# Kernel optimization log

Measured on AMD Instinct MI355X. Metric: run time of the kernel, lower is better.

Reference implementation:

```python
import jax, jax.numpy as jnp
import numpy as np

NEG_SLOPE = 0.01  # torch.nn.LeakyReLU default


def setup_inputs() -> dict:
    key = jax.random.key(0)
    ks = jax.random.split(key, 9)
    B, S, F1, F2, N, M, E, L = 2, 256, 512, 512, 20000, 2, 320000, 3
    x = jax.random.normal(ks[0], (B, S, F1), dtype=jnp.float32)
    nodes = jax.random.normal(ks[1], (N, M, F2), dtype=jnp.float32)
    edge_index = jax.random.randint(ks[2], (2, E), 0, N, dtype=jnp.int32)
    Wp = jax.random.normal(ks[3], (F1, F2), dtype=jnp.float32) * 0.02  # torch Linear weight [out,in]
    bp = jax.random.normal(ks[4], (F1,), dtype=jnp.float32) * 0.02
    gcn_W = jax.random.normal(ks[5], (L, S, S), dtype=jnp.float32) * 0.05  # stored as [in,out]
    gcn_b = jax.random.normal(ks[6], (L, S), dtype=jnp.float32) * 0.02
    w_bp = jax.random.normal(ks[7], (S,), dtype=jnp.float32) * 0.05
    b_bp = jax.random.normal(ks[8], (1,), dtype=jnp.float32) * 0.02
    return {"x": x, "nodes": nodes, "edge_index": edge_index, "Wp": Wp, "bp": bp,
            "gcn_W": gcn_W, "gcn_b": gcn_b, "w_bp": w_bp, "b_bp": b_bp}


def reference(x, nodes, edge_index, Wp, bp, gcn_W, gcn_b, w_bp, b_bp):
    # Eval mode: dropout layers are identity.
    N = nodes.shape[0]
    L = gcn_W.shape[0]
    proj = nodes @ Wp.T + bp                         # [N, M, F1]
    score = jnp.einsum('bsk,nmk->bsn', x, proj)      # sum over M and F1 -> [B, S, N]
    h = score.transpose(0, 2, 1)                     # beliefs [B, N, S]

    # GCN normalization with self-loops: D^{-1/2} (A + I) D^{-1/2}
    src, dst = edge_index[0], edge_index[1]
    loop = jnp.arange(N, dtype=edge_index.dtype)
    row = jnp.concatenate([src, loop])               # message sources
    col = jnp.concatenate([dst, loop])               # message targets
    deg = jnp.zeros((N,), dtype=h.dtype).at[col].add(1.0)
    dinv = deg ** -0.5                               # deg >= 1 due to self-loops
    norm = dinv[row] * dinv[col]                     # [E+N]

    for l in range(L):
        hw = h @ gcn_W[l]                            # [B, N, S]
        msg = hw[:, row, :] * norm[None, :, None]    # gather + scale
        agg = jnp.zeros_like(hw).at[:, col, :].add(msg) + gcn_b[l]
        h = jax.nn.leaky_relu(agg, NEG_SLOPE)

    # belief_projection: Linear(S, 1) then squeeze -> [B, N]
    return h @ w_bp + b_bp[0]
```

## Files before the change

kernel.cpp:

```cpp
#include <hip/hip_runtime.h>
#include <cstddef>
#include <cstdint>

#define NN 20000

typedef short frag16 __attribute__((ext_vector_type(8)));
typedef float f32x4 __attribute__((ext_vector_type(4)));

__device__ inline unsigned short f32_to_bf16(float f) {
    uint32_t u = __float_as_uint(f);
    u += 0x7FFFu + ((u >> 16) & 1u);
    return (unsigned short)(u >> 16);
}

__device__ inline float4 dec4(uint2 v) {
    float4 r;
    r.x = __uint_as_float(v.x << 16);
    r.y = __uint_as_float(v.x & 0xffff0000u);
    r.z = __uint_as_float(v.y << 16);
    r.w = __uint_as_float(v.y & 0xffff0000u);
    return r;
}

__global__ __launch_bounds__(256) void prep(
    const float* __restrict__ nodes, const float* __restrict__ x,
    const float* __restrict__ gcn_W, const float* __restrict__ bp,
    const int* __restrict__ src, const int* __restrict__ dst,
    unsigned short* __restrict__ nsum16, unsigned short* __restrict__ WT,
    float* __restrict__ Tf, float* __restrict__ cvec,
    int* __restrict__ cnt, int* __restrict__ csr, int E)
{
    __shared__ __align__(16) char shmem[8704];
    const int blk = blockIdx.x, tid = threadIdx.x;
    const int eb = (E + 255) >> 8;

    if (blk < eb) {
        int e = blk * 256 + tid;
        if (e < E) {
            int d = dst[e];
            int pos = atomicAdd(&cnt[d], 1);
            if (pos < 64) csr[(d << 6) + pos] = src[e];
        }
    } else if (blk < eb + 64) {
        float* As = (float*)shmem;
        float* Bs = As + 1024;
        int t = blk - eb;
        int b = t >> 5, rem = t & 31;
        int s0 = (rem >> 3) * 64, f0 = (rem & 7) * 64;
        const float* W1 = gcn_W;
        const float* xb = x + (size_t)b * 256 * 512;
        int kk = tid >> 4, c4 = (tid & 15) << 2;
        int tm = tid >> 4, tn = tid & 15;
        float acc[4][4] = {};
        for (int k0 = 0; k0 < 256; k0 += 16) {
            float4 av = *(const float4*)(W1 + (size_t)(k0 + kk) * 256 + s0 + c4);
            float4 bv = *(const float4*)(xb + (size_t)(k0 + kk) * 512 + f0 + c4);
            __syncthreads();
            *(float4*)&As[kk * 64 + c4] = av;
            *(float4*)&Bs[kk * 64 + c4] = bv;
            __syncthreads();
            #pragma unroll
            for (int k = 0; k < 16; ++k) {
                float a[4], bb[4];
                *(float4*)a  = *(const float4*)&As[k * 64 + (tm << 2)];
                *(float4*)bb = *(const float4*)&Bs[k * 64 + (tn << 2)];
                #pragma unroll
                for (int i = 0; i < 4; ++i)
                    #pragma unroll
                    for (int j = 0; j < 4; ++j) acc[i][j] += a[i] * bb[j];
            }
        }
        #pragma unroll
        for (int i = 0; i < 4; ++i) {
            int row = b * 256 + s0 + (tm << 2) + i;
            *(float4*)(Tf + (size_t)row * 512 + f0 + (tn << 2)) =
                make_float4(acc[i][0], acc[i][1], acc[i][2], acc[i][3]);
        }
    } else if (blk < eb + 64 + 2512) {
        int g = (blk - eb - 64) * 256 + tid;
        int n = g >> 5, c = (g & 31) << 4;
        uint4 o0, o1;
        if (n < NN) {
            const float* r0 = nodes + (size_t)n * 1024 + c;
            const float* r1 = r0 + 512;
            float4 a0 = *(const float4*)(r0 + 0),  a1 = *(const float4*)(r0 + 4);
            float4 a2 = *(const float4*)(r0 + 8),  a3 = *(const float4*)(r0 + 12);
            float4 b0 = *(const float4*)(r1 + 0),  b1 = *(const float4*)(r1 + 4);
            float4 b2 = *(const float4*)(r1 + 8),  b3 = *(const float4*)(r1 + 12);
            o0.x = ((uint32_t)f32_to_bf16(a0.y + b0.y) << 16) | f32_to_bf16(a0.x + b0.x);
            o0.y = ((uint32_t)f32_to_bf16(a0.w + b0.w) << 16) | f32_to_bf16(a0.z + b0.z);
            o0.z = ((uint32_t)f32_to_bf16(a1.y + b1.y) << 16) | f32_to_bf16(a1.x + b1.x);
            o0.w = ((uint32_t)f32_to_bf16(a1.w + b1.w) << 16) | f32_to_bf16(a1.z + b1.z);
            o1.x = ((uint32_t)f32_to_bf16(a2.y + b2.y) << 16) | f32_to_bf16(a2.x + b2.x);
            o1.y = ((uint32_t)f32_to_bf16(a2.w + b2.w) << 16) | f32_to_bf16(a2.z + b2.z);
            o1.z = ((uint32_t)f32_to_bf16(a3.y + b3.y) << 16) | f32_to_bf16(a3.x + b3.x);
            o1.w = ((uint32_t)f32_to_bf16(a3.w + b3.w) << 16) | f32_to_bf16(a3.z + b3.z);
        } else {
            o0 = make_uint4(0, 0, 0, 0); o1 = o0;
        }
        *(uint4*)(nsum16 + (size_t)n * 512 + c) = o0;
        *(uint4*)(nsum16 + (size_t)n * 512 + c + 8) = o1;
    } else if (blk < eb + 64 + 2512 + 32) {
        unsigned short (*tsh)[68] = (unsigned short(*)[68])shmem;
        int t = blk - eb - 64 - 2512;
        int l = t >> 4, rem = t & 15;
        int c0 = (rem & 3) * 64, r0 = (rem >> 2) * 64;
        const float* inp = gcn_W + (size_t)(l + 1) * 65536;
        unsigned short* outp = WT + (size_t)l * 65536;
        int tx = tid & 15, ty = tid >> 4;
        #pragma unroll
        for (int rr = 0; rr < 4; ++rr) {
            int r = ty * 4 + rr;
            float4 v = *(const float4*)(inp + (size_t)(r0 + r) * 256 + c0 + tx * 4);
            tsh[tx * 4 + 0][r] = f32_to_bf16(v.x);
            tsh[tx * 4 + 1][r] = f32_to_bf16(v.y);
            tsh[tx * 4 + 2][r] = f32_to_bf16(v.z);
            tsh[tx * 4 + 3][r] = f32_to_bf16(v.w);
        }
        __syncthreads();
        #pragma unroll
        for (int cc = 0; cc < 4; ++cc) {
            int c = ty * 4 + cc;
            ushort4 o = *(ushort4*)&tsh[c][tx * 4];
            *(ushort4*)(outp + (size_t)(c0 + c) * 256 + r0 + tx * 4) = o;
        }
    } else {
        int row = (blk - eb - 64 - 2512 - 32) * 4 + (tid >> 6);
        int lane = tid & 63;
        const float* xr = x + (size_t)row * 512;
        float s = 0.f;
        #pragma unroll
        for (int k = 0; k < 512; k += 64) s += xr[k + lane] * bp[k + lane];
        #pragma unroll
        for (int off = 32; off; off >>= 1) s += __shfl_down(s, off);
        if (lane == 0) cvec[row] = 2.0f * s;
    }
}

__global__ __launch_bounds__(256) void mid(
    const float* __restrict__ Tf, const float* __restrict__ Wp,
    const float* __restrict__ gcn_W, const float* __restrict__ cvec,
    unsigned short* __restrict__ Ub, float* __restrict__ cb2)
{
    const int blk = blockIdx.x, tid = threadIdx.x;
    if (blk >= 64) {
        int idx = (blk - 64) * 256 + tid;
        int b = idx >> 8, s = idx & 255;
        float sum = 0.f;
        for (int sp = 0; sp < 256; ++sp)
            sum += gcn_W[(size_t)sp * 256 + s] * cvec[b * 256 + sp];
        cb2[idx] = sum;
        return;
    }
    __shared__ float As[16][68];
    __shared__ float Bs[16][64];
    int bm = (blk >> 3) * 64, bn = (blk & 7) * 64;
    int arow = tid >> 2, acol = (tid & 3) << 2;
    int brow = tid >> 4, bcol = (tid & 15) << 2;
    int tm = tid >> 4, tn = tid & 15;
    float acc[4][4] = {};
    for (int k0 = 0; k0 < 512; k0 += 16) {
        float4 av = *(const float4*)(Tf + (size_t)(bm + arow) * 512 + k0 + acol);
        float4 bv = *(const float4*)(Wp + (size_t)(k0 + brow) * 512 + bn + bcol);
        __syncthreads();
        As[acol + 0][arow] = av.x; As[acol + 1][arow] = av.y;
        As[acol + 2][arow] = av.z; As[acol + 3][arow] = av.w;
        *(float4*)&Bs[brow][bcol] = bv;
        __syncthreads();
        #pragma unroll
        for (int k = 0; k < 16; ++k) {
            float a[4], b[4];
            *(float4*)a = *(const float4*)&As[k][tm << 2];
            *(float4*)b = *(const float4*)&Bs[k][tn << 2];
            #pragma unroll
            for (int i = 0; i < 4; ++i)
                #pragma unroll
                for (int j = 0; j < 4; ++j) acc[i][j] += a[i] * b[j];
        }
    }
    #pragma unroll
    for (int i = 0; i < 4; ++i) {
        int row = bm + (tm << 2) + i;
        ushort4 o;
        o.x = f32_to_bf16(acc[i][0]); o.y = f32_to_bf16(acc[i][1]);
        o.z = f32_to_bf16(acc[i][2]); o.w = f32_to_bf16(acc[i][3]);
        *(ushort4*)(Ub + (size_t)row * 512 + bn + (tn << 2)) = o;
    }
}

__global__ __launch_bounds__(256) void mgemm(
    const unsigned short* __restrict__ A, const unsigned short* __restrict__ BT,
    int K, int N, int mode,
    const float* __restrict__ cb2, const int* __restrict__ cnt,
    unsigned short* __restrict__ C)
{
    __shared__ __align__(16) unsigned short As[128 * 32];
    __shared__ __align__(16) unsigned short Bs[128 * 32];
    const int bm = blockIdx.y * 128, bn = blockIdx.x * 128;
    const int tid = threadIdx.x;
    const int lane = tid & 63, w = tid >> 6;
    const int wm = (w >> 1) << 6, wn = (w & 1) << 6;
    const int r = lane & 15, q = lane >> 4;

    f32x4 acc[4][4] = {};

    for (int k0 = 0; k0 < K; k0 += 32) {
        __syncthreads();
        #pragma unroll
        for (int t = 0; t < 2; ++t) {
            int c = t * 256 + w * 64 + lane;
            int row = c >> 2, col = (c & 3) << 3;
            __builtin_amdgcn_global_load_lds(
                (const __attribute__((address_space(1))) void*)(A + (size_t)(bm + row) * K + k0 + col),
                (__attribute__((address_space(3))) void*)(As + (size_t)(t * 256 + w * 64) * 8),
                16, 0, 0);
            __builtin_amdgcn_global_load_lds(
                (const __attribute__((address_space(1))) void*)(BT + (size_t)(bn + row) * K + k0 + col),
                (__attribute__((address_space(3))) void*)(Bs + (size_t)(t * 256 + w * 64) * 8),
                16, 0, 0);
        }
        __syncthreads();
        frag16 af[4], bf[4];
        #pragma unroll
        for (int i = 0; i < 4; ++i)
            af[i] = *(const frag16*)(As + ((wm + i * 16 + r) << 5) + (q << 3));
        #pragma unroll
        for (int j = 0; j < 4; ++j)
            bf[j] = *(const frag16*)(Bs + ((wn + j * 16 + r) << 5) + (q << 3));
        #pragma unroll
        for (int i = 0; i < 4; ++i)
            #pragma unroll
            for (int j = 0; j < 4; ++j)
                acc[i][j] = __builtin_amdgcn_mfma_f32_16x16x32_bf16(af[i], bf[j], acc[i][j], 0, 0, 0);
    }

    #pragma unroll
    for (int i = 0; i < 4; ++i) {
        #pragma unroll
        for (int rg = 0; rg < 4; ++rg) {
            int m = bm + wm + i * 16 + (q << 2) + rg;
            float sc;
            int b2 = 0, node = m;
            if (mode == 1) {
                int nc = m > NN - 1 ? NN - 1 : m;
                sc = rsqrtf((float)cnt[nc] + 1.0f);
            } else {
                b2 = m >= NN;
                node = m - b2 * NN;
                int nc = node > NN - 1 ? NN - 1 : node;
                sc = rsqrtf((float)cnt[nc] + 1.0f);
                if (node > 20095) node = 20095;
            }
            #pragma unroll
            for (int j = 0; j < 4; ++j) {
                int n = bn + wn + j * 16 + r;
                if (mode == 1) {
                    float v = (acc[i][j][rg] + cb2[n]) * sc;
                    C[(size_t)m * 512 + n] = f32_to_bf16(v);
                } else {
                    float v = acc[i][j][rg] * sc;
                    C[(size_t)node * 512 + (b2 << 8) + n] = f32_to_bf16(v);
                }
            }
        }
    }
}

__global__ __launch_bounds__(256) void aggregate_s(
    const unsigned short* __restrict__ hw, const int* __restrict__ cnt,
    const int* __restrict__ csr, const float* __restrict__ bias,
    unsigned short* __restrict__ hout,
    const float* __restrict__ w_bp, const float* __restrict__ b_bp,
    float* __restrict__ out)
{
    int n = blockIdx.x * 4 + (threadIdx.x >> 6);
    int b = blockIdx.y;
    int lane = threadIdx.x & 63;
    const unsigned short* rowp = hw + (b << 8) + (lane << 2);

    int deg = cnt[n]; if (deg > 64) deg = 64;
    int myidx = csr[(n << 6) + lane];

    float4 acc = dec4(*(const uint2*)(rowp + (size_t)n * 512));
    int e = 0;
    for (; e + 8 <= deg; e += 8) {
        int s0 = __shfl(myidx, e + 0), s1 = __shfl(myidx, e + 1);
        int s2 = __shfl(myidx, e + 2), s3 = __shfl(myidx, e + 3);
        int s4 = __shfl(myidx, e + 4), s5 = __shfl(myidx, e + 5);
        int s6 = __shfl(myidx, e + 6), s7 = __shfl(myidx, e + 7);
        uint2 u0 = *(const uint2*)(rowp + (size_t)s0 * 512);
        uint2 u1 = *(const uint2*)(rowp + (size_t)s1 * 512);
        uint2 u2 = *(const uint2*)(rowp + (size_t)s2 * 512);
        uint2 u3 = *(const uint2*)(rowp + (size_t)s3 * 512);
        uint2 u4 = *(const uint2*)(rowp + (size_t)s4 * 512);
        uint2 u5 = *(const uint2*)(rowp + (size_t)s5 * 512);
        uint2 u6 = *(const uint2*)(rowp + (size_t)s6 * 512);
        uint2 u7 = *(const uint2*)(rowp + (size_t)s7 * 512);
        float4 f0 = dec4(u0), f1 = dec4(u1), f2 = dec4(u2), f3 = dec4(u3);
        float4 f4 = dec4(u4), f5 = dec4(u5), f6 = dec4(u6), f7 = dec4(u7);
        acc.x += ((f0.x + f1.x) + (f2.x + f3.x)) + ((f4.x + f5.x) + (f6.x + f7.x));
        acc.y += ((f0.y + f1.y) + (f2.y + f3.y)) + ((f4.y + f5.y) + (f6.y + f7.y));
        acc.z += ((f0.z + f1.z) + (f2.z + f3.z)) + ((f4.z + f5.z) + (f6.z + f7.z));
        acc.w += ((f0.w + f1.w) + (f2.w + f3.w)) + ((f4.w + f5.w) + (f6.w + f7.w));
    }
    if (e + 4 <= deg) {
        int s0 = __shfl(myidx, e + 0), s1 = __shfl(myidx, e + 1);
        int s2 = __shfl(myidx, e + 2), s3 = __shfl(myidx, e + 3);
        uint2 u0 = *(const uint2*)(rowp + (size_t)s0 * 512);
        uint2 u1 = *(const uint2*)(rowp + (size_t)s1 * 512);
        uint2 u2 = *(const uint2*)(rowp + (size_t)s2 * 512);
        uint2 u3 = *(const uint2*)(rowp + (size_t)s3 * 512);
        float4 f0 = dec4(u0), f1 = dec4(u1), f2 = dec4(u2), f3 = dec4(u3);
        acc.x += (f0.x + f1.x) + (f2.x + f3.x);
        acc.y += (f0.y + f1.y) + (f2.y + f3.y);
        acc.z += (f0.z + f1.z) + (f2.z + f3.z);
        acc.w += (f0.w + f1.w) + (f2.w + f3.w);
        e += 4;
    }
    for (; e < deg; ++e) {
        int s0 = __shfl(myidx, e);
        float4 f = dec4(*(const uint2*)(rowp + (size_t)s0 * 512));
        acc.x += f.x; acc.y += f.y; acc.z += f.z; acc.w += f.w;
    }

    float dn = rsqrtf((float)deg + 1.0f);
    int s = lane << 2;
    float4 bl = *(const float4*)(bias + s);
    float4 v;
    v.x = fmaf(dn, acc.x, bl.x); v.y = fmaf(dn, acc.y, bl.y);
    v.z = fmaf(dn, acc.z, bl.z); v.w = fmaf(dn, acc.w, bl.w);
    v.x = v.x > 0.f ? v.x : 0.01f * v.x;
    v.y = v.y > 0.f ? v.y : 0.01f * v.y;
    v.z = v.z > 0.f ? v.z : 0.01f * v.z;
    v.w = v.w > 0.f ? v.w : 0.01f * v.w;

    if (out) {
        float4 w4 = *(const float4*)(w_bp + s);
        float sum = v.x * w4.x + v.y * w4.y + v.z * w4.z + v.w * w4.w;
        #pragma unroll
        for (int off = 32; off; off >>= 1) sum += __shfl_xor(sum, off);
        if (lane == 0) out[b * NN + n] = sum + b_bp[0];
    } else {
        uint2 o;
        o.x = ((uint32_t)f32_to_bf16(v.y) << 16) | f32_to_bf16(v.x);
        o.y = ((uint32_t)f32_to_bf16(v.w) << 16) | f32_to_bf16(v.z);
        *(uint2*)(hout + ((size_t)(b * NN + n)) * 256 + s) = o;
    }
}

extern "C" void kernel_launch(void* const* d_in, const int* in_sizes, int n_in,
                              void* d_out, int out_size, void* d_ws, size_t ws_size,
                              hipStream_t stream) {
    const float* x     = (const float*)d_in[0];
    const float* nodes = (const float*)d_in[1];
    const int*   eidx  = (const int*)d_in[2];
    const float* Wp    = (const float*)d_in[3];
    const float* bp    = (const float*)d_in[4];
    const float* gcn_W = (const float*)d_in[5];
    const float* gcn_b = (const float*)d_in[6];
    const float* w_bp  = (const float*)d_in[7];
    const float* b_bp  = (const float*)d_in[8];
    const int E = in_sizes[2] / 2;

    char* w = (char*)d_ws;
    auto alloc = [&](size_t bytes) { char* p = w; w += (bytes + 255) & ~(size_t)255; return p; };
    unsigned short* nsum16 = (unsigned short*)alloc((size_t)20096 * 512 * 2);
    unsigned short* hw16   = (unsigned short*)alloc((size_t)20096 * 512 * 2);
    unsigned short* hA     = (unsigned short*)alloc((size_t)40192 * 256 * 2);
    unsigned short* hB     = (unsigned short*)alloc((size_t)40192 * 256 * 2);
    float* Tf  = (float*)alloc((size_t)512 * 512 * 4);
    unsigned short* Ub = (unsigned short*)alloc((size_t)512 * 512 * 2);
    unsigned short* WT = (unsigned short*)alloc((size_t)2 * 256 * 256 * 2);
    float* cvec = (float*)alloc(512 * 4);
    float* cb2  = (float*)alloc(512 * 4);
    int*   cnt  = (int*)alloc((size_t)NN * 4);
    int*   csr  = (int*)alloc((size_t)NN * 64 * 4);

    hipMemsetAsync(cnt, 0, (size_t)NN * 4, stream);

    const int cntBlks = (E + 255) / 256;
    prep<<<cntBlks + 64 + 2512 + 32 + 128, 256, 0, stream>>>(
        nodes, x, gcn_W, bp, eidx, eidx + E, nsum16, WT, Tf, cvec, cnt, csr, E);
    mid<<<66, 256, 0, stream>>>(Tf, Wp, gcn_W, cvec, Ub, cb2);

    mgemm<<<dim3(4, 157), 256, 0, stream>>>(nsum16, Ub, 512, 512, 1, cb2, cnt, hw16);

    aggregate_s<<<dim3(5000, 2), 256, 0, stream>>>(hw16, cnt, csr, gcn_b + 0, hA,
                                                   w_bp, b_bp, nullptr);
    mgemm<<<dim3(2, 313), 256, 0, stream>>>(hA, WT, 256, 256, 2, nullptr, cnt, hw16);
    aggregate_s<<<dim3(5000, 2), 256, 0, stream>>>(hw16, cnt, csr, gcn_b + 256, hB,
                                                   w_bp, b_bp, nullptr);
    mgemm<<<dim3(2, 313), 256, 0, stream>>>(hB, WT + 65536, 256, 256, 2, nullptr, cnt, hw16);
    aggregate_s<<<dim3(5000, 2), 256, 0, stream>>>(hw16, cnt, csr, gcn_b + 512, nullptr,
                                                   w_bp, b_bp, (float*)d_out);
}
```

Measured before the change: 376.5 us.

## Fuse all stages into one persistent kernel with software grid barriers

Replaces the eight separate launches (prep, mid, three GEMMs, three aggregations) with a single persistent kernel of 768 blocks that loops over each stage's work items and separates stages with atomic-counter grid barriers. The goal is to remove per-launch overhead and the idle tail between dependent kernels. The cost is barrier spin latency and reduced flexibility in occupancy per stage. Correctness depends on all 768 blocks being co-resident (3 per CU via launch bounds), and the barrier's spin cap could silently break synchronisation if that does not hold.

```diff
diff --git a/kernel.cpp b/kernel.cpp
--- a/kernel.cpp
+++ b/kernel.cpp
@@ -3,6 +3,7 @@
 #include <cstdint>
 
 #define NN 20000
+#define GRID 768
 
 typedef short frag16 __attribute__((ext_vector_type(8)));
 typedef float f32x4 __attribute__((ext_vector_type(4)));
@@ -22,181 +23,31 @@
     return r;
 }
 
-__global__ __launch_bounds__(256) void prep(
-    const float* __restrict__ nodes, const float* __restrict__ x,
-    const float* __restrict__ gcn_W, const float* __restrict__ bp,
-    const int* __restrict__ src, const int* __restrict__ dst,
-    unsigned short* __restrict__ nsum16, unsigned short* __restrict__ WT,
-    float* __restrict__ Tf, float* __restrict__ cvec,
-    int* __restrict__ cnt, int* __restrict__ csr, int E)
+__device__ inline void gridbar(int* barcnt, int* barflag, int idx) {
+    __syncthreads();
+    if (threadIdx.x == 0) {
+        __threadfence();
+        if (atomicAdd(&barcnt[idx], 1) == GRID - 1) {
+            atomicExch(&barflag[idx], 1);
+        } else {
+            int spins = 0;
+            while (atomicAdd(&barflag[idx], 0) == 0 && spins < (1 << 24)) {
+                __builtin_amdgcn_s_sleep(8);
+                ++spins;
+            }
+        }
+        __threadfence();
+    }
+    __syncthreads();
+}
+
+__device__ void mgemm_body(char* smem,
+    const unsigned short* __restrict__ A, const unsigned short* __restrict__ BT,
+    int K, int mode, const float* __restrict__ cb2, const int* __restrict__ cnt,
+    unsigned short* __restrict__ C, int bm, int bn)
 {
-    __shared__ __align__(16) char shmem[8704];
-    const int blk = blockIdx.x, tid = threadIdx.x;
-    const int eb = (E + 255) >> 8;
-
-    if (blk < eb) {
-        int e = blk * 256 + tid;
-        if (e < E) {
-            int d = dst[e];
-            int pos = atomicAdd(&cnt[d], 1);
-            if (pos < 64) csr[(d << 6) + pos] = src[e];
-        }
-    } else if (blk < eb + 64) {
-        float* As = (float*)shmem;
-        float* Bs = As + 1024;
-        int t = blk - eb;
-        int b = t >> 5, rem = t & 31;
-        int s0 = (rem >> 3) * 64, f0 = (rem & 7) * 64;
-        const float* W1 = gcn_W;
-        const float* xb = x + (size_t)b * 256 * 512;
-        int kk = tid >> 4, c4 = (tid & 15) << 2;
-        int tm = tid >> 4, tn = tid & 15;
-        float acc[4][4] = {};
-        for (int k0 = 0; k0 < 256; k0 += 16) {
-            float4 av = *(const float4*)(W1 + (size_t)(k0 + kk) * 256 + s0 + c4);
-            float4 bv = *(const float4*)(xb + (size_t)(k0 + kk) * 512 + f0 + c4);
-            __syncthreads();
-            *(float4*)&As[kk * 64 + c4] = av;
-            *(float4*)&Bs[kk * 64 + c4] = bv;
-            __syncthreads();
-            #pragma unroll
-            for (int k = 0; k < 16; ++k) {
-                float a[4], bb[4];
-                *(float4*)a  = *(const float4*)&As[k * 64 + (tm << 2)];
-                *(float4*)bb = *(const float4*)&Bs[k * 64 + (tn << 2)];
-                #pragma unroll
-                for (int i = 0; i < 4; ++i)
-                    #pragma unroll
-                    for (int j = 0; j < 4; ++j) acc[i][j] += a[i] * bb[j];
-            }
-        }
-        #pragma unroll
-        for (int i = 0; i < 4; ++i) {
-            int row = b * 256 + s0 + (tm << 2) + i;
-            *(float4*)(Tf + (size_t)row * 512 + f0 + (tn << 2)) =
-                make_float4(acc[i][0], acc[i][1], acc[i][2], acc[i][3]);
-        }
-    } else if (blk < eb + 64 + 2512) {
-        int g = (blk - eb - 64) * 256 + tid;
-        int n = g >> 5, c = (g & 31) << 4;
-        uint4 o0, o1;
-        if (n < NN) {
-            const float* r0 = nodes + (size_t)n * 1024 + c;
-            const float* r1 = r0 + 512;
-            float4 a0 = *(const float4*)(r0 + 0),  a1 = *(const float4*)(r0 + 4);
-            float4 a2 = *(const float4*)(r0 + 8),  a3 = *(const float4*)(r0 + 12);
-            float4 b0 = *(const float4*)(r1 + 0),  b1 = *(const float4*)(r1 + 4);
-            float4 b2 = *(const float4*)(r1 + 8),  b3 = *(const float4*)(r1 + 12);
-            o0.x = ((uint32_t)f32_to_bf16(a0.y + b0.y) << 16) | f32_to_bf16(a0.x + b0.x);
-            o0.y = ((uint32_t)f32_to_bf16(a0.w + b0.w) << 16) | f32_to_bf16(a0.z + b0.z);
-            o0.z = ((uint32_t)f32_to_bf16(a1.y + b1.y) << 16) | f32_to_bf16(a1.x + b1.x);
-            o0.w = ((uint32_t)f32_to_bf16(a1.w + b1.w) << 16) | f32_to_bf16(a1.z + b1.z);
-            o1.x = ((uint32_t)f32_to_bf16(a2.y + b2.y) << 16) | f32_to_bf16(a2.x + b2.x);
-            o1.y = ((uint32_t)f32_to_bf16(a2.w + b2.w) << 16) | f32_to_bf16(a2.z + b2.z);
-            o1.z = ((uint32_t)f32_to_bf16(a3.y + b3.y) << 16) | f32_to_bf16(a3.x + b3.x);
-            o1.w = ((uint32_t)f32_to_bf16(a3.w + b3.w) << 16) | f32_to_bf16(a3.z + b3.z);
-        } else {
-            o0 = make_uint4(0, 0, 0, 0); o1 = o0;
-        }
-        *(uint4*)(nsum16 + (size_t)n * 512 + c) = o0;
-        *(uint4*)(nsum16 + (size_t)n * 512 + c + 8) = o1;
-    } else if (blk < eb + 64 + 2512 + 32) {
-        unsigned short (*tsh)[68] = (unsigned short(*)[68])shmem;
-        int t = blk - eb - 64 - 2512;
-        int l = t >> 4, rem = t & 15;
-        int c0 = (rem & 3) * 64, r0 = (rem >> 2) * 64;
-        const float* inp = gcn_W + (size_t)(l + 1) * 65536;
-        unsigned short* outp = WT + (size_t)l * 65536;
-        int tx = tid & 15, ty = tid >> 4;
-        #pragma unroll
-        for (int rr = 0; rr < 4; ++rr) {
-            int r = ty * 4 + rr;
-            float4 v = *(const float4*)(inp + (size_t)(r0 + r) * 256 + c0 + tx * 4);
-            tsh[tx * 4 + 0][r] = f32_to_bf16(v.x);
-            tsh[tx * 4 + 1][r] = f32_to_bf16(v.y);
-            tsh[tx * 4 + 2][r] = f32_to_bf16(v.z);
-            tsh[tx * 4 + 3][r] = f32_to_bf16(v.w);
-        }
-        __syncthreads();
-        #pragma unroll
-        for (int cc = 0; cc < 4; ++cc) {
-            int c = ty * 4 + cc;
-            ushort4 o = *(ushort4*)&tsh[c][tx * 4];
-            *(ushort4*)(outp + (size_t)(c0 + c) * 256 + r0 + tx * 4) = o;
-        }
-    } else {
-        int row = (blk - eb - 64 - 2512 - 32) * 4 + (tid >> 6);
-        int lane = tid & 63;
-        const float* xr = x + (size_t)row * 512;
-        float s = 0.f;
-        #pragma unroll
-        for (int k = 0; k < 512; k += 64) s += xr[k + lane] * bp[k + lane];
-        #pragma unroll
-        for (int off = 32; off; off >>= 1) s += __shfl_down(s, off);
-        if (lane == 0) cvec[row] = 2.0f * s;
-    }
-}
-
-__global__ __launch_bounds__(256) void mid(
-    const float* __restrict__ Tf, const float* __restrict__ Wp,
-    const float* __restrict__ gcn_W, const float* __restrict__ cvec,
-    unsigned short* __restrict__ Ub, float* __restrict__ cb2)
-{
-    const int blk = blockIdx.x, tid = threadIdx.x;
-    if (blk >= 64) {
-        int idx = (blk - 64) * 256 + tid;
-        int b = idx >> 8, s = idx & 255;
-        float sum = 0.f;
-        for (int sp = 0; sp < 256; ++sp)
-            sum += gcn_W[(size_t)sp * 256 + s] * cvec[b * 256 + sp];
-        cb2[idx] = sum;
-        return;
-    }
-    __shared__ float As[16][68];
-    __shared__ float Bs[16][64];
-    int bm = (blk >> 3) * 64, bn = (blk & 7) * 64;
-    int arow = tid >> 2, acol = (tid & 3) << 2;
-    int brow = tid >> 4, bcol = (tid & 15) << 2;
-    int tm = tid >> 4, tn = tid & 15;
-    float acc[4][4] = {};
-    for (int k0 = 0; k0 < 512; k0 += 16) {
-        float4 av = *(const float4*)(Tf + (size_t)(bm + arow) * 512 + k0 + acol);
-        float4 bv = *(const float4*)(Wp + (size_t)(k0 + brow) * 512 + bn + bcol);
-        __syncthreads();
-        As[acol + 0][arow] = av.x; As[acol + 1][arow] = av.y;
-        As[acol + 2][arow] = av.z; As[acol + 3][arow] = av.w;
-        *(float4*)&Bs[brow][bcol] = bv;
-        __syncthreads();
-        #pragma unroll
-        for (int k = 0; k < 16; ++k) {
-            float a[4], b[4];
-            *(float4*)a = *(const float4*)&As[k][tm << 2];
-            *(float4*)b = *(const float4*)&Bs[k][tn << 2];
-            #pragma unroll
-            for (int i = 0; i < 4; ++i)
-                #pragma unroll
-                for (int j = 0; j < 4; ++j) acc[i][j] += a[i] * b[j];
-        }
-    }
-    #pragma unroll
-    for (int i = 0; i < 4; ++i) {
-        int row = bm + (tm << 2) + i;
-        ushort4 o;
-        o.x = f32_to_bf16(acc[i][0]); o.y = f32_to_bf16(acc[i][1]);
-        o.z = f32_to_bf16(acc[i][2]); o.w = f32_to_bf16(acc[i][3]);
-        *(ushort4*)(Ub + (size_t)row * 512 + bn + (tn << 2)) = o;
-    }
-}
-
-__global__ __launch_bounds__(256) void mgemm(
-    const unsigned short* __restrict__ A, const unsigned short* __restrict__ BT,
-    int K, int N, int mode,
-    const float* __restrict__ cb2, const int* __restrict__ cnt,
-    unsigned short* __restrict__ C)
-{
-    __shared__ __align__(16) unsigned short As[128 * 32];
-    __shared__ __align__(16) unsigned short Bs[128 * 32];
-    const int bm = blockIdx.y * 128, bn = blockIdx.x * 128;
+    unsigned short* As = (unsigned short*)smem;
+    unsigned short* Bs = As + 128 * 32;
     const int tid = threadIdx.x;
     const int lane = tid & 63, w = tid >> 6;
     const int wm = (w >> 1) << 6, wn = (w & 1) << 6;
@@ -266,15 +117,13 @@
     }
 }
 
-__global__ __launch_bounds__(256) void aggregate_s(
+__device__ void agg_body(
     const unsigned short* __restrict__ hw, const int* __restrict__ cnt,
     const int* __restrict__ csr, const float* __restrict__ bias,
     unsigned short* __restrict__ hout,
     const float* __restrict__ w_bp, const float* __restrict__ b_bp,
-    float* __restrict__ out)
+    float* __restrict__ out, int n, int b)
 {
-    int n = blockIdx.x * 4 + (threadIdx.x >> 6);
-    int b = blockIdx.y;
     int lane = threadIdx.x & 63;
     const unsigned short* rowp = hw + (b << 8) + (lane << 2);
 
@@ -348,6 +197,217 @@
     }
 }
 
+__global__ __launch_bounds__(256, 3) void persist(
+    const float* __restrict__ nodes, const float* __restrict__ x,
+    const float* __restrict__ Wp, const float* __restrict__ gcn_W,
+    const float* __restrict__ bp, const int* __restrict__ src,
+    const int* __restrict__ dst, const float* __restrict__ gcn_b,
+    const float* __restrict__ w_bp, const float* __restrict__ b_bp,
+    unsigned short* __restrict__ nsum16, unsigned short* __restrict__ hw16,
+    unsigned short* __restrict__ hA, unsigned short* __restrict__ hB,
+    float* __restrict__ Tf, unsigned short* __restrict__ Ub,
+    unsigned short* __restrict__ WT, float* __restrict__ cvec,
+    float* __restrict__ cb2, int* __restrict__ cnt,
+    int* __restrict__ barcnt, int* __restrict__ barflag,
+    int* __restrict__ csr, float* __restrict__ out, int E)
+{
+    __shared__ __align__(16) char smem[16896];
+    const int tid = threadIdx.x;
+    const int eb = (E + 255) >> 8;
+    const int prepN = eb + 64 + 2512 + 32 + 128;
+
+    for (int blk = blockIdx.x; blk < prepN; blk += GRID) {
+        if (blk < eb) {
+            int e = blk * 256 + tid;
+            if (e < E) {
+                int d = dst[e];
+                int pos = atomicAdd(&cnt[d], 1);
+                if (pos < 64) csr[(d << 6) + pos] = src[e];
+            }
+        } else if (blk < eb + 64) {
+            float* As = (float*)smem;
+            float* Bs = As + 1024;
+            int t = blk - eb;
+            int b = t >> 5, rem = t & 31;
+            int s0 = (rem >> 3) * 64, f0 = (rem & 7) * 64;
+            const float* W1 = gcn_W;
+            const float* xb = x + (size_t)b * 256 * 512;
+            int kk = tid >> 4, c4 = (tid & 15) << 2;
+            int tm = tid >> 4, tn = tid & 15;
+            float acc[4][4] = {};
+            for (int k0 = 0; k0 < 256; k0 += 16) {
+                float4 av = *(const float4*)(W1 + (size_t)(k0 + kk) * 256 + s0 + c4);
+                float4 bv = *(const float4*)(xb + (size_t)(k0 + kk) * 512 + f0 + c4);
+                __syncthreads();
+                *(float4*)&As[kk * 64 + c4] = av;
+                *(float4*)&Bs[kk * 64 + c4] = bv;
+                __syncthreads();
+                #pragma unroll
+                for (int k = 0; k < 16; ++k) {
+                    float a[4], bb[4];
+                    *(float4*)a  = *(const float4*)&As[k * 64 + (tm << 2)];
+                    *(float4*)bb = *(const float4*)&Bs[k * 64 + (tn << 2)];
+                    #pragma unroll
+                    for (int i = 0; i < 4; ++i)
+                        #pragma unroll
+                        for (int j = 0; j < 4; ++j) acc[i][j] += a[i] * bb[j];
+                }
+            }
+            #pragma unroll
+            for (int i = 0; i < 4; ++i) {
+                int row = b * 256 + s0 + (tm << 2) + i;
+                *(float4*)(Tf + (size_t)row * 512 + f0 + (tn << 2)) =
+                    make_float4(acc[i][0], acc[i][1], acc[i][2], acc[i][3]);
+            }
+            __syncthreads();
+        } else if (blk < eb + 64 + 2512) {
+            int g = (blk - eb - 64) * 256 + tid;
+            int n = g >> 5, c = (g & 31) << 4;
+            uint4 o0, o1;
+            if (n < NN) {
+                const float* r0 = nodes + (size_t)n * 1024 + c;
+                const float* r1 = r0 + 512;
+                float4 a0 = *(const float4*)(r0 + 0),  a1 = *(const float4*)(r0 + 4);
+                float4 a2 = *(const float4*)(r0 + 8),  a3 = *(const float4*)(r0 + 12);
+                float4 b0 = *(const float4*)(r1 + 0),  b1 = *(const float4*)(r1 + 4);
+                float4 b2 = *(const float4*)(r1 + 8),  b3 = *(const float4*)(r1 + 12);
+                o0.x = ((uint32_t)f32_to_bf16(a0.y + b0.y) << 16) | f32_to_bf16(a0.x + b0.x);
+                o0.y = ((uint32_t)f32_to_bf16(a0.w + b0.w) << 16) | f32_to_bf16(a0.z + b0.z);
+                o0.z = ((uint32_t)f32_to_bf16(a1.y + b1.y) << 16) | f32_to_bf16(a1.x + b1.x);
+                o0.w = ((uint32_t)f32_to_bf16(a1.w + b1.w) << 16) | f32_to_bf16(a1.z + b1.z);
+                o1.x = ((uint32_t)f32_to_bf16(a2.y + b2.y) << 16) | f32_to_bf16(a2.x + b2.x);
+                o1.y = ((uint32_t)f32_to_bf16(a2.w + b2.w) << 16) | f32_to_bf16(a2.z + b2.z);
+                o1.z = ((uint32_t)f32_to_bf16(a3.y + b3.y) << 16) | f32_to_bf16(a3.x + b3.x);
+                o1.w = ((uint32_t)f32_to_bf16(a3.w + b3.w) << 16) | f32_to_bf16(a3.z + b3.z);
+            } else {
+                o0 = make_uint4(0, 0, 0, 0); o1 = o0;
+            }
+            *(uint4*)(nsum16 + (size_t)n * 512 + c) = o0;
+            *(uint4*)(nsum16 + (size_t)n * 512 + c + 8) = o1;
+        } else if (blk < eb + 64 + 2512 + 32) {
+            unsigned short (*tsh)[68] = (unsigned short(*)[68])smem;
+            int t = blk - eb - 64 - 2512;
+            int l = t >> 4, rem = t & 15;
+            int c0 = (rem & 3) * 64, r0 = (rem >> 2) * 64;
+            const float* inp = gcn_W + (size_t)(l + 1) * 65536;
+            unsigned short* outp = WT + (size_t)l * 65536;
+            int tx = tid & 15, ty = tid >> 4;
+            __syncthreads();
+            #pragma unroll
+            for (int rr = 0; rr < 4; ++rr) {
+                int r = ty * 4 + rr;
+                float4 v = *(const float4*)(inp + (size_t)(r0 + r) * 256 + c0 + tx * 4);
+                tsh[tx * 4 + 0][r] = f32_to_bf16(v.x);
+                tsh[tx * 4 + 1][r] = f32_to_bf16(v.y);
+                tsh[tx * 4 + 2][r] = f32_to_bf16(v.z);
+                tsh[tx * 4 + 3][r] = f32_to_bf16(v.w);
+            }
+            __syncthreads();
+            #pragma unroll
+            for (int cc = 0; cc < 4; ++cc) {
+                int c = ty * 4 + cc;
+                ushort4 o = *(ushort4*)&tsh[c][tx * 4];
+                *(ushort4*)(outp + (size_t)(c0 + c) * 256 + r0 + tx * 4) = o;
+            }
+            __syncthreads();
+        } else {
+            int row = (blk - eb - 64 - 2512 - 32) * 4 + (tid >> 6);
+            int lane = tid & 63;
+            const float* xr = x + (size_t)row * 512;
+            float s = 0.f;
+            #pragma unroll
+            for (int k = 0; k < 512; k += 64) s += xr[k + lane] * bp[k + lane];
+            #pragma unroll
+            for (int off = 32; off; off >>= 1) s += __shfl_down(s, off);
+            if (lane == 0) cvec[row] = 2.0f * s;
+        }
+    }
+    gridbar(barcnt, barflag, 0);
+
+    for (int blk = blockIdx.x; blk < 66; blk += GRID) {
+        if (blk >= 64) {
+            int idx = (blk - 64) * 256 + tid;
+            int b = idx >> 8, s = idx & 255;
+            float sum = 0.f;
+            for (int sp = 0; sp < 256; ++sp)
+                sum += gcn_W[(size_t)sp * 256 + s] * cvec[b * 256 + sp];
+            cb2[idx] = sum;
+        } else {
+            float* As = (float*)smem;
+            float* Bs = As + 16 * 68;
+            int bm = (blk >> 3) * 64, bn = (blk & 7) * 64;
+            int arow = tid >> 2, acol = (tid & 3) << 2;
+            int brow = tid >> 4, bcol = (tid & 15) << 2;
+            int tm = tid >> 4, tn = tid & 15;
+            float acc[4][4] = {};
+            for (int k0 = 0; k0 < 512; k0 += 16) {
+                float4 av = *(const float4*)(Tf + (size_t)(bm + arow) * 512 + k0 + acol);
+                float4 bv = *(const float4*)(Wp + (size_t)(k0 + brow) * 512 + bn + bcol);
+                __syncthreads();
+                As[(acol + 0) * 68 + arow] = av.x; As[(acol + 1) * 68 + arow] = av.y;
+                As[(acol + 2) * 68 + arow] = av.z; As[(acol + 3) * 68 + arow] = av.w;
+                *(float4*)&Bs[brow * 64 + bcol] = bv;
+                __syncthreads();
+                #pragma unroll
+                for (int k = 0; k < 16; ++k) {
+                    float a[4], b[4];
+                    *(float4*)a = *(const float4*)&As[k * 68 + (tm << 2)];
+                    *(float4*)b = *(const float4*)&Bs[k * 64 + (tn << 2)];
+                    #pragma unroll
+                    for (int i = 0; i < 4; ++i)
+                        #pragma unroll
+                        for (int j = 0; j < 4; ++j) acc[i][j] += a[i] * b[j];
+                }
+            }
+            #pragma unroll
+            for (int i = 0; i < 4; ++i) {
+                int row = bm + (tm << 2) + i;
+                ushort4 o;
+                o.x = f32_to_bf16(acc[i][0]); o.y = f32_to_bf16(acc[i][1]);
+                o.z = f32_to_bf16(acc[i][2]); o.w = f32_to_bf16(acc[i][3]);
+                *(ushort4*)(Ub + (size_t)row * 512 + bn + (tn << 2)) = o;
+            }
+            __syncthreads();
+        }
+    }
+    gridbar(barcnt, barflag, 1);
+
+    for (int it = blockIdx.x; it < 628; it += GRID)
+        mgemm_body(smem, nsum16, Ub, 512, 1, cb2, cnt, hw16,
+                   (it >> 2) * 128, (it & 3) * 128);
+    gridbar(barcnt, barflag, 2);
+
+    for (int it = blockIdx.x; it < 10000; it += GRID) {
+        int b = it >= 5000;
+        int n = (it - b * 5000) * 4 + (tid >> 6);
+        agg_body(hw16, cnt, csr, gcn_b + 0, hA, w_bp, b_bp, nullptr, n, b);
+    }
+    gridbar(barcnt, barflag, 3);
+
+    for (int it = blockIdx.x; it < 626; it += GRID)
+        mgemm_body(smem, hA, WT, 256, 2, nullptr, cnt, hw16,
+                   (it >> 1) * 128, (it & 1) * 128);
+    gridbar(barcnt, barflag, 4);
+
+    for (int it = blockIdx.x; it < 10000; it += GRID) {
+        int b = it >= 5000;
+        int n = (it - b * 5000) * 4 + (tid >> 6);
+        agg_body(hw16, cnt, csr, gcn_b + 256, hB, w_bp, b_bp, nullptr, n, b);
+    }
+    gridbar(barcnt, barflag, 5);
+
+    for (int it = blockIdx.x; it < 626; it += GRID)
+        mgemm_body(smem, hB, WT + 65536, 256, 2, nullptr, cnt, hw16,
+                   (it >> 1) * 128, (it & 1) * 128);
+    gridbar(barcnt, barflag, 6);
+
+    for (int it = blockIdx.x; it < 10000; it += GRID) {
+        int b = it >= 5000;
+        int n = (it - b * 5000) * 4 + (tid >> 6);
+        agg_body(hw16, cnt, csr, gcn_b + 512, nullptr, w_bp, b_bp, out, n, b);
+    }
+}
+
 extern "C" void kernel_launch(void* const* d_in, const int* in_sizes, int n_in,
                               void* d_out, int out_size, void* d_ws, size_t ws_size,
                               hipStream_t stream) {
@@ -373,24 +433,15 @@
     unsigned short* WT = (unsigned short*)alloc((size_t)2 * 256 * 256 * 2);
     float* cvec = (float*)alloc(512 * 4);
     float* cb2  = (float*)alloc(512 * 4);
-    int*   cnt  = (int*)alloc((size_t)NN * 4);
+    int*   cnt  = (int*)alloc((size_t)NN * 4 + 256);
     int*   csr  = (int*)alloc((size_t)NN * 64 * 4);
-
-    hipMemsetAsync(cnt, 0, (size_t)NN * 4, stream);
-
-    const int cntBlks = (E + 255) / 256;
-    prep<<<cntBlks + 64 + 2512 + 32 + 128, 256, 0, stream>>>(
-        nodes, x, gcn_W, bp, eidx, eidx + E, nsum16, WT, Tf, cvec, cnt, csr, E);
-    mid<<<66, 256, 0, stream>>>(Tf, Wp, gcn_W, cvec, Ub, cb2);
-
-    mgemm<<<dim3(4, 157), 256, 0, stream>>>(nsum16, Ub, 512, 512, 1, cb2, cnt, hw16);
-
-    aggregate_s<<<dim3(5000, 2), 256, 0, stream>>>(hw16, cnt, csr, gcn_b + 0, hA,
-                                                   w_bp, b_bp, nullptr);
-    mgemm<<<dim3(2, 313), 256, 0, stream>>>(hA, WT, 256, 256, 2, nullptr, cnt, hw16);
-    aggregate_s<<<dim3(5000, 2), 256, 0, stream>>>(hw16, cnt, csr, gcn_b + 256, hB,
-                                                   w_bp, b_bp, nullptr);
-    mgemm<<<dim3(2, 313), 256, 0, stream>>>(hB, WT + 65536, 256, 256, 2, nullptr, cnt, hw16);
-    aggregate_s<<<dim3(5000, 2), 256, 0, stream>>>(hw16, cnt, csr, gcn_b + 512, nullptr,
-                                                   w_bp, b_bp, (float*)d_out);
-}
+    int* barcnt  = cnt + NN;
+    int* barflag = cnt + NN + 16;
+
+    hipMemsetAsync(cnt, 0, (size_t)NN * 4 + 256, stream);
+
+    persist<<<GRID, 256, 0, stream>>>(
+        nodes, x, Wp, gcn_W, bp, eidx, eidx + E, gcn_b, w_bp, b_bp,
+        nsum16, hw16, hA, hB, Tf, Ub, WT, cvec, cb2,
+        cnt, barcnt, barflag, csr, (float*)d_out, E);
+}
```

Result: slower. 966.6 us (+156.7%).
